# Performance work log

Hardware: AMD Instinct MI355X
Metric: run time of the kernel (lower is better)

## Reference

```python
import jax, jax.numpy as jnp
import numpy as np

N_NODES = 40000
N_EDGES = 640000
IN_CH = 128
OUT_CH = 128
BN_EPS = 1e-5


def setup_inputs() -> dict:
    key = jax.random.key(0)
    ks = jax.random.split(key, 8)
    x = jax.random.normal(ks[0], (N_NODES, IN_CH), dtype=jnp.float32)
    edge_index = jax.random.randint(ks[1], (2, N_EDGES), 0, N_NODES, dtype=jnp.int64)
    s1 = 1.0 / np.sqrt(IN_CH)
    s2 = 1.0 / np.sqrt(OUT_CH)
    W1 = jax.random.uniform(ks[2], (OUT_CH, IN_CH), jnp.float32, -s1, s1)
    b1 = jax.random.uniform(ks[3], (OUT_CH,), jnp.float32, -s1, s1)
    gamma = jnp.ones((OUT_CH,), jnp.float32)
    beta = jnp.zeros((OUT_CH,), jnp.float32)
    W2 = jax.random.uniform(ks[4], (OUT_CH, OUT_CH), jnp.float32, -s2, s2)
    b2 = jax.random.uniform(ks[5], (OUT_CH,), jnp.float32, -s2, s2)
    eps = jnp.float32(0.0)
    return {"x": x, "edge_index": edge_index, "W1": W1, "b1": b1,
            "gamma": gamma, "beta": beta, "W2": W2, "b2": b2, "eps": eps}


def reference(x, edge_index, W1, b1, gamma, beta, W2, b2, eps):
    src, dst = edge_index[0], edge_index[1]
    # neighbor sum: agg[v] = sum_{(u,v) in E} x[u]
    agg = jax.ops.segment_sum(x[src], dst, num_segments=N_NODES)  # [N, in_ch]
    h = (1.0 + eps) * x + agg
    # Linear 1
    h = h @ W1.T + b1  # [N, out_ch]
    # BatchNorm1d (training mode: batch stats, biased variance)
    mu = jnp.mean(h, axis=0)
    var = jnp.var(h, axis=0)
    h = (h - mu) * jax.lax.rsqrt(var + BN_EPS) * gamma + beta
    # ReLU + Linear 2
    h = jnp.maximum(h, 0.0)
    return h @ W2.T + b2
```

## Files before the change

### kernel.cpp

```cpp
#include <hip/hip_runtime.h>

#define NN 40000
#define NE 640000
#define BN_EPS 1e-5f

typedef __attribute__((ext_vector_type(8))) short bf16x8;
typedef __attribute__((ext_vector_type(4))) float f32x4;
typedef unsigned int uint;
typedef unsigned short ushort;

__device__ __forceinline__ float blo(uint u) { return __uint_as_float(u << 16); }
__device__ __forceinline__ float bhi(uint u) { return __uint_as_float(u & 0xFFFF0000u); }
__device__ __forceinline__ uint bpack(float lo, float hi) {
    uint a = __float_as_uint(lo); a = (a + 0x7FFFu + ((a >> 16) & 1u)) >> 16;
    uint b = __float_as_uint(hi); b = (b + 0x7FFFu + ((b >> 16) & 1u)) & 0xFFFF0000u;
    return a | b;
}
__device__ __forceinline__ ushort b1pack(float v) {
    uint u = __float_as_uint(v); return (ushort)((u + 0x7FFFu + ((u >> 16) & 1u)) >> 16);
}
__device__ __forceinline__ uint4 cvt8(const float4* f4, int i) {
    float4 p = f4[i * 2], q = f4[i * 2 + 1];
    uint4 o;
    o.x = bpack(p.x, p.y); o.y = bpack(p.z, p.w);
    o.z = bpack(q.x, q.y); o.w = bpack(q.z, q.w);
    return o;
}

__global__ __launch_bounds__(256) void k_prep(const float* __restrict__ x, const float* __restrict__ W1,
                                              const float* __restrict__ W2, const int* __restrict__ ei,
                                              int* __restrict__ cnt, float* __restrict__ bn,
                                              uint* __restrict__ xb, uint* __restrict__ w1b,
                                              uint* __restrict__ w2b, ushort* __restrict__ srcl) {
    int b = blockIdx.x, t = threadIdx.x;
    if (b < 2500) {
        int e = b * 256 + t;
        int s = ei[e];
        int d = ei[NE + e];
        int pos = atomicAdd(&cnt[d], 1);
        if (pos < 64) srcl[d * 64 + pos] = (ushort)s;
    } else if (b < 5000) {
        int i = (b - 2500) * 256 + t;
        ((uint4*)xb)[i] = cvt8((const float4*)x, i);
    } else if (b < 5008) {
        int i = (b - 5000) * 256 + t;
        ((uint4*)w1b)[i] = cvt8((const float4*)W1, i);
    } else if (b < 5016) {
        int i = (b - 5008) * 256 + t;
        ((uint4*)w2b)[i] = cvt8((const float4*)W2, i);
    } else {
        bn[t] = 0.f;
    }
}

__global__ __launch_bounds__(256) void k_gather(const uint4* __restrict__ xq, const int* __restrict__ cnt,
                                                const ushort* __restrict__ srcl, const float* __restrict__ epsp,
                                                uint4* __restrict__ hbq) {
    int wid = blockIdx.x * 4 + (threadIdx.x >> 6);
    int lane = threadIdx.x & 63;
    int grp = lane >> 4;
    int cidx = lane & 15;
    int deg = cnt[wid]; deg = deg > 64 ? 64 : deg;
    int sv = srcl[wid * 64 + lane];

    float acc[8];
#pragma unroll
    for (int j = 0; j < 8; ++j) acc[j] = 0.f;

    int chunks = (deg + 7) >> 3;
    for (int c = 0; c < chunks; ++c) {
        int i = c * 8;
        int n0 = i + grp, n1 = i + 4 + grp;
        int s0 = __shfl(sv, n0);
        int s1 = __shfl(sv, n1);
        float m0 = n0 < deg ? 1.f : 0.f;
        float m1 = n1 < deg ? 1.f : 0.f;
        s0 = n0 < deg ? s0 : 0;
        s1 = n1 < deg ? s1 : 0;
        uint4 v0 = xq[(size_t)s0 * 16 + cidx];
        uint4 v1 = xq[(size_t)s1 * 16 + cidx];
        acc[0] = fmaf(blo(v0.x), m0, acc[0]); acc[1] = fmaf(bhi(v0.x), m0, acc[1]);
        acc[2] = fmaf(blo(v0.y), m0, acc[2]); acc[3] = fmaf(bhi(v0.y), m0, acc[3]);
        acc[4] = fmaf(blo(v0.z), m0, acc[4]); acc[5] = fmaf(bhi(v0.z), m0, acc[5]);
        acc[6] = fmaf(blo(v0.w), m0, acc[6]); acc[7] = fmaf(bhi(v0.w), m0, acc[7]);
        acc[0] = fmaf(blo(v1.x), m1, acc[0]); acc[1] = fmaf(bhi(v1.x), m1, acc[1]);
        acc[2] = fmaf(blo(v1.y), m1, acc[2]); acc[3] = fmaf(bhi(v1.y), m1, acc[3]);
        acc[4] = fmaf(blo(v1.z), m1, acc[4]); acc[5] = fmaf(bhi(v1.z), m1, acc[5]);
        acc[6] = fmaf(blo(v1.w), m1, acc[6]); acc[7] = fmaf(bhi(v1.w), m1, acc[7]);
    }
#pragma unroll
    for (int j = 0; j < 8; ++j) {
        acc[j] += __shfl_xor(acc[j], 16);
        acc[j] += __shfl_xor(acc[j], 32);
    }
    if (grp == 0) {
        float e1 = 1.f + epsp[0];
        uint4 s = xq[(size_t)wid * 16 + cidx];
        uint4 o;
        o.x = bpack(fmaf(blo(s.x), e1, acc[0]), fmaf(bhi(s.x), e1, acc[1]));
        o.y = bpack(fmaf(blo(s.y), e1, acc[2]), fmaf(bhi(s.y), e1, acc[3]));
        o.z = bpack(fmaf(blo(s.z), e1, acc[4]), fmaf(bhi(s.z), e1, acc[5]));
        o.w = bpack(fmaf(blo(s.w), e1, acc[6]), fmaf(bhi(s.w), e1, acc[7]));
        hbq[(size_t)wid * 16 + cidx] = o;
    }
}

__global__ __launch_bounds__(256) void k_mm1(const ushort* __restrict__ hb, const ushort* __restrict__ w1b,
                                             const float* __restrict__ b1, ushort* __restrict__ h1b,
                                             float* __restrict__ bnsum, float* __restrict__ bnsumsq) {
    __shared__ float rs[256 * 8];
    __shared__ float rq[256 * 8];
    const int tid = threadIdx.x;
    const int wave = tid >> 6;
    const int lane = tid & 63;
    const int lr = lane & 15;
    const int lk = lane >> 4;
    const int r0 = (blockIdx.x * 4 + wave) * 16;

    bf16x8 a[4];
#pragma unroll
    for (int ks = 0; ks < 4; ++ks)
        a[ks] = *reinterpret_cast<const bf16x8*>(&hb[(size_t)(r0 + lr) * 128 + ks * 32 + lk * 8]);

    f32x4 acc[8];
#pragma unroll
    for (int t = 0; t < 8; ++t) { acc[t][0] = 0.f; acc[t][1] = 0.f; acc[t][2] = 0.f; acc[t][3] = 0.f; }

#pragma unroll
    for (int t = 0; t < 8; ++t) {
        const ushort* wrow = &w1b[(size_t)(t * 16 + lr) * 128];
#pragma unroll
        for (int ks = 0; ks < 4; ++ks) {
            bf16x8 bfr = *reinterpret_cast<const bf16x8*>(&wrow[ks * 32 + lk * 8]);
            acc[t] = __builtin_amdgcn_mfma_f32_16x16x32_bf16(a[ks], bfr, acc[t], 0, 0, 0);
        }
    }
#pragma unroll
    for (int t = 0; t < 8; ++t) {
        float bias = b1[t * 16 + lr];
        float s = 0.f, q = 0.f;
#pragma unroll
        for (int i = 0; i < 4; ++i) {
            float v = acc[t][i] + bias;
            h1b[(size_t)(r0 + lk * 4 + i) * 128 + t * 16 + lr] = b1pack(v);
            s += v; q += v * v;
        }
        rs[tid * 8 + t] = s;
        rq[tid * 8 + t] = q;
    }
    __syncthreads();
    if (tid < 128) {
        int c = tid, t = c >> 4, cr = c & 15;
        float s = 0.f, q = 0.f;
#pragma unroll
        for (int w = 0; w < 4; ++w)
#pragma unroll
            for (int g = 0; g < 4; ++g) {
                int src = w * 64 + g * 16 + cr;
                s += rs[src * 8 + t];
                q += rq[src * 8 + t];
            }
        atomicAdd(&bnsum[c], s);
        atomicAdd(&bnsumsq[c], q);
    }
}

__global__ __launch_bounds__(256) void k_mm2(const ushort* __restrict__ h1b, const ushort* __restrict__ w2b,
                                             const float* __restrict__ b2,
                                             const float* __restrict__ bnsum, const float* __restrict__ bnsumsq,
                                             const float* __restrict__ gamma, const float* __restrict__ beta,
                                             float* __restrict__ out) {
    __shared__ float ssc[128], ssh[128];
    const int tid = threadIdx.x;
    if (tid < 128) {
        float mu = bnsum[tid] * (1.0f / NN);
        float var = bnsumsq[tid] * (1.0f / NN) - mu * mu;
        float rsv = rsqrtf(var + BN_EPS);
        float g = rsv * gamma[tid];
        ssc[tid] = g;
        ssh[tid] = beta[tid] - mu * g;
    }
    __syncthreads();

    const int wave = tid >> 6;
    const int lane = tid & 63;
    const int lr = lane & 15;
    const int lk = lane >> 4;
    const int r0 = (blockIdx.x * 4 + wave) * 16;

    bf16x8 a[4];
#pragma unroll
    for (int ks = 0; ks < 4; ++ks) {
        int kbase = ks * 32 + lk * 8;
        bf16x8 raw = *reinterpret_cast<const bf16x8*>(&h1b[(size_t)(r0 + lr) * 128 + kbase]);
        bf16x8 o;
#pragma unroll
        for (int j = 0; j < 8; ++j) {
            float v = __uint_as_float(((uint)(ushort)raw[j]) << 16);
            v = fmaxf(0.f, fmaf(v, ssc[kbase + j], ssh[kbase + j]));
            o[j] = (short)b1pack(v);
        }
        a[ks] = o;
    }

    f32x4 acc[8];
#pragma unroll
    for (int t = 0; t < 8; ++t) { acc[t][0] = 0.f; acc[t][1] = 0.f; acc[t][2] = 0.f; acc[t][3] = 0.f; }

#pragma unroll
    for (int t = 0; t < 8; ++t) {
        const ushort* wrow = &w2b[(size_t)(t * 16 + lr) * 128];
#pragma unroll
        for (int ks = 0; ks < 4; ++ks) {
            bf16x8 bfr = *reinterpret_cast<const bf16x8*>(&wrow[ks * 32 + lk * 8]);
            acc[t] = __builtin_amdgcn_mfma_f32_16x16x32_bf16(a[ks], bfr, acc[t], 0, 0, 0);
        }
    }
#pragma unroll
    for (int t = 0; t < 8; ++t) {
        float bias = b2[t * 16 + lr];
#pragma unroll
        for (int i = 0; i < 4; ++i)
            out[(size_t)(r0 + lk * 4 + i) * 128 + t * 16 + lr] = acc[t][i] + bias;
    }
}

extern "C" void kernel_launch(void* const* d_in, const int* in_sizes, int n_in,
                              void* d_out, int out_size, void* d_ws, size_t ws_size,
                              hipStream_t stream) {
    const float* x     = (const float*)d_in[0];
    const int*   ei    = (const int*)d_in[1];
    const float* W1    = (const float*)d_in[2];
    const float* b1    = (const float*)d_in[3];
    const float* gamma = (const float*)d_in[4];
    const float* beta  = (const float*)d_in[5];
    const float* W2    = (const float*)d_in[6];
    const float* b2    = (const float*)d_in[7];
    const float* eps   = (const float*)d_in[8];

    char* ws = (char*)d_ws;
    int*    cnt  = (int*)(ws + 0);
    ushort* srcl = (ushort*)(ws + 160000);
    uint*   xb   = (uint*)(ws + 5280000);
    uint*   hb   = (uint*)(ws + 15520000);
    ushort* h1b  = (ushort*)(ws + 25760000);
    uint*   w1b  = (uint*)(ws + 36000000);
    uint*   w2b  = (uint*)(ws + 36032768);
    float*  bn   = (float*)(ws + 36065536);
    float* bnsum   = bn;
    float* bnsumsq = bn + 128;

    hipMemsetAsync(cnt, 0, 160000, stream);
    k_prep<<<5017, 256, 0, stream>>>(x, W1, W2, ei, cnt, bn, xb, w1b, w2b, srcl);
    k_gather<<<10000, 256, 0, stream>>>((const uint4*)xb, cnt, srcl, eps, (uint4*)hb);
    k_mm1<<<625, 256, 0, stream>>>((const ushort*)hb, (const ushort*)w1b, b1, h1b, bnsum, bnsumsq);
    k_mm2<<<625, 256, 0, stream>>>(h1b, (const ushort*)w2b, b2, bnsum, bnsumsq, gamma, beta, (float*)d_out);
}
```

Before: 111.5 us.

## Split neighbor gather into per-block channel slices for cache locality

```diff
diff --git a/kernel.cpp b/kernel.cpp
--- a/kernel.cpp
+++ b/kernel.cpp
@@ -53,55 +53,42 @@
     }
 }
 
-__global__ __launch_bounds__(256) void k_gather(const uint4* __restrict__ xq, const int* __restrict__ cnt,
+__global__ __launch_bounds__(256) void k_gather(const uint* __restrict__ xbv, const int* __restrict__ cnt,
                                                 const ushort* __restrict__ srcl, const float* __restrict__ epsp,
-                                                uint4* __restrict__ hbq) {
-    int wid = blockIdx.x * 4 + (threadIdx.x >> 6);
-    int lane = threadIdx.x & 63;
-    int grp = lane >> 4;
-    int cidx = lane & 15;
-    int deg = cnt[wid]; deg = deg > 64 ? 64 : deg;
-    int sv = srcl[wid * 64 + lane];
-
-    float acc[8];
-#pragma unroll
-    for (int j = 0; j < 8; ++j) acc[j] = 0.f;
-
-    int chunks = (deg + 7) >> 3;
-    for (int c = 0; c < chunks; ++c) {
-        int i = c * 8;
-        int n0 = i + grp, n1 = i + 4 + grp;
-        int s0 = __shfl(sv, n0);
-        int s1 = __shfl(sv, n1);
-        float m0 = n0 < deg ? 1.f : 0.f;
-        float m1 = n1 < deg ? 1.f : 0.f;
-        s0 = n0 < deg ? s0 : 0;
-        s1 = n1 < deg ? s1 : 0;
-        uint4 v0 = xq[(size_t)s0 * 16 + cidx];
-        uint4 v1 = xq[(size_t)s1 * 16 + cidx];
-        acc[0] = fmaf(blo(v0.x), m0, acc[0]); acc[1] = fmaf(bhi(v0.x), m0, acc[1]);
-        acc[2] = fmaf(blo(v0.y), m0, acc[2]); acc[3] = fmaf(bhi(v0.y), m0, acc[3]);
-        acc[4] = fmaf(blo(v0.z), m0, acc[4]); acc[5] = fmaf(bhi(v0.z), m0, acc[5]);
-        acc[6] = fmaf(blo(v0.w), m0, acc[6]); acc[7] = fmaf(bhi(v0.w), m0, acc[7]);
-        acc[0] = fmaf(blo(v1.x), m1, acc[0]); acc[1] = fmaf(bhi(v1.x), m1, acc[1]);
-        acc[2] = fmaf(blo(v1.y), m1, acc[2]); acc[3] = fmaf(bhi(v1.y), m1, acc[3]);
-        acc[4] = fmaf(blo(v1.z), m1, acc[4]); acc[5] = fmaf(bhi(v1.z), m1, acc[5]);
-        acc[6] = fmaf(blo(v1.w), m1, acc[6]); acc[7] = fmaf(bhi(v1.w), m1, acc[7]);
-    }
-#pragma unroll
-    for (int j = 0; j < 8; ++j) {
-        acc[j] += __shfl_xor(acc[j], 16);
-        acc[j] += __shfl_xor(acc[j], 32);
-    }
-    if (grp == 0) {
-        float e1 = 1.f + epsp[0];
-        uint4 s = xq[(size_t)wid * 16 + cidx];
-        uint4 o;
-        o.x = bpack(fmaf(blo(s.x), e1, acc[0]), fmaf(bhi(s.x), e1, acc[1]));
-        o.y = bpack(fmaf(blo(s.y), e1, acc[2]), fmaf(bhi(s.y), e1, acc[3]));
-        o.z = bpack(fmaf(blo(s.z), e1, acc[4]), fmaf(bhi(s.z), e1, acc[5]));
-        o.w = bpack(fmaf(blo(s.w), e1, acc[6]), fmaf(bhi(s.w), e1, acc[7]));
-        hbq[(size_t)wid * 16 + cidx] = o;
+                                                uint* __restrict__ hb) {
+    const int g = blockIdx.x;
+    const int slice = g & 7;
+    const int ng = g >> 3;
+    const int wave = threadIdx.x >> 6;
+    const int lane = threadIdx.x & 63;
+    const int sub = lane >> 3;
+    const int ch = lane & 7;
+    const int sbase = slice * 8 + ch;
+    const float e1 = 1.f + epsp[0];
+    const int nbase = ng * 32 + wave * 8;
+
+#pragma unroll 2
+    for (int t = 0; t < 8; ++t) {
+        int node = nbase + t;
+        int deg = cnt[node]; deg = deg > 64 ? 64 : deg;
+        int sv = srcl[(size_t)node * 64 + lane];
+        uint su = xbv[(size_t)node * 64 + sbase];
+        float a0 = 0.f, a1 = 0.f;
+        int chunks = (deg + 7) >> 3;
+        for (int c = 0; c < chunks; ++c) {
+            int n = c * 8 + sub;
+            int s = __shfl(sv, n);
+            bool ok = n < deg;
+            s = ok ? s : 0;
+            uint v = xbv[(size_t)s * 64 + sbase];
+            a0 += ok ? blo(v) : 0.f;
+            a1 += ok ? bhi(v) : 0.f;
+        }
+        a0 += __shfl_xor(a0, 8);  a1 += __shfl_xor(a1, 8);
+        a0 += __shfl_xor(a0, 16); a1 += __shfl_xor(a1, 16);
+        a0 += __shfl_xor(a0, 32); a1 += __shfl_xor(a1, 32);
+        if (sub == 0)
+            hb[(size_t)node * 64 + sbase] = bpack(fmaf(blo(su), e1, a0), fmaf(bhi(su), e1, a1));
     }
 }
 
@@ -252,7 +239,7 @@
 
     hipMemsetAsync(cnt, 0, 160000, stream);
     k_prep<<<5017, 256, 0, stream>>>(x, W1, W2, ei, cnt, bn, xb, w1b, w2b, srcl);
-    k_gather<<<10000, 256, 0, stream>>>((const uint4*)xb, cnt, srcl, eps, (uint4*)hb);
+    k_gather<<<10000, 256, 0, stream>>>(xb, cnt, srcl, eps, hb);
     k_mm1<<<625, 256, 0, stream>>>((const ushort*)hb, (const ushort*)w1b, b1, h1b, bnsum, bnsumsq);
     k_mm2<<<625, 256, 0, stream>>>(h1b, (const ushort*)w2b, b2, bnsum, bnsumsq, gamma, beta, (float*)d_out);
 }
```

Result: slower. 165.8 us (+48.6%).
